# Optimization experiments

Measured on AMD Instinct MI355X. Metric: run time of the kernel, lower is better.

The kernel has to match this reference:

```python
import jax, jax.numpy as jnp
import numpy as np

D_STATE = 2048
D_INPUT = 64
KERNEL_SIZE = 16384


def setup_inputs() -> dict:
    key = jax.random.key(0)
    k_rad, k_ph, k_w = jax.random.split(key, 3)
    # Discrete diagonal state matrix: complex eigenvalues with radius in
    # [strong_stability, weak_stability] = [0.9, 0.999], uniform phase.
    radius = 0.9 + 0.099 * jax.random.uniform(k_rad, (D_STATE,), dtype=jnp.float32)
    phase = 2.0 * jnp.pi * jax.random.uniform(k_ph, (D_STATE,), dtype=jnp.float32)
    A = jnp.stack([radius * jnp.cos(phase), radius * jnp.sin(phase)], axis=-1)  # (P, 2) view_as_real
    # Reservoir uniform complex matrix W: (H, P) complex stored as (H, P, 2) real
    W = jax.random.uniform(k_w, (D_INPUT, D_STATE, 2), dtype=jnp.float32, minval=-1.0, maxval=1.0)
    return {"A": A, "W": W, "kernel_size": KERNEL_SIZE}


def reference(A, W, kernel_size):
    # view_as_complex
    Ac = A[:, 0] + 1j * A[:, 1]          # (P,)
    Wc = W[..., 0] + 1j * W[..., 1]      # (H, P)
    powers = jnp.arange(kernel_size, dtype=jnp.float32)  # (L,)
    # Vandermonde[j, l] = A[j]^l, computed stably in log-space (|A| < 1)
    vandermonde = jnp.exp(jnp.log(Ac)[:, None] * powers[None, :])  # (P, L) complex
    kernel = jnp.einsum('hp,pl->hl', Wc, vandermonde)  # (H, L) complex
    return kernel
```

## Files before the change

kernel.cpp:

```cpp
#include <hip/hip_runtime.h>
#include <hip/hip_bf16.h>
#include <stdint.h>

#define P 2048
#define HN 64
#define L 16384
#define BN 64
#define KTW 16

typedef __bf16 bf16_t;
typedef bf16_t bf16x8 __attribute__((ext_vector_type(8)));
typedef float f32x16 __attribute__((ext_vector_type(16)));

__device__ __forceinline__ float2 cmul(float2 a, float2 b) {
    return make_float2(a.x * b.x - a.y * b.y, a.x * b.y + a.y * b.x);
}

__device__ __forceinline__ uint32_t packbf(float2 v) {
    union { __hip_bfloat162 v; uint32_t u; } cv;
    cv.v = __float22bfloat162_rn(make_float2(v.x, v.y));
    return cv.u;
}

__global__ void mv_prep(const float* __restrict__ Win,
                        const float* __restrict__ Ain,
                        uint4* __restrict__ wexp,
                        float2* __restrict__ tcol,
                        float2* __restrict__ a32) {
    int gid = blockIdx.x * 256 + threadIdx.x;
    {
        int lane = gid & 63;
        int mt = (gid >> 6) & 1;
        int q = (gid >> 7) & 1;
        int kt = gid >> 8;
        int m = mt * 32 + (lane & 31);
        int p0 = kt * 16 + q * 8 + (lane >> 5) * 4;
        const float4* wp = (const float4*)(Win + (size_t)(m * P + p0) * 2);
        float4 f0 = wp[0], f1 = wp[1];
        float re[4] = {f0.x, f0.z, f1.x, f1.z};
        float im[4] = {f0.y, f0.w, f1.y, f1.w};
        uint32_t o[4];
#pragma unroll
        for (int j = 0; j < 4; ++j)
            o[j] = packbf(make_float2(re[j], -im[j]));
        wexp[gid] = make_uint4(o[0], o[1], o[2], o[3]);
    }
    {
        int p = gid >> 4;
        int e = gid & 15;
        float2 a = *(const float2*)(Ain + 2 * p);
        float2 a2 = cmul(a, a);
        float2 r = make_float2(1.f, 0.f);
        float2 sq = a2;
#pragma unroll
        for (int b = 0; b < 4; ++b) {
            if ((e >> b) & 1) r = cmul(r, sq);
            sq = cmul(sq, sq);
        }
        float2 ro = cmul(r, a);
        tcol[(size_t)p * 32 + 2 * e] = r;
        tcol[(size_t)p * 32 + 2 * e + 1] = ro;
        if (e == 15) a32[p] = cmul(ro, a);
    }
}

struct StepRegs {
    uint4 a[2][2];
    float2 tv[8];
};

__global__ void __launch_bounds__(512, 2) mv_main(
    const float* __restrict__ Ain,
    const uint4* __restrict__ wexp,
    const float2* __restrict__ Tcol,
    const float2* __restrict__ A32,
    float* __restrict__ out) {
    __shared__ __align__(16) float ldsp[8192];

    const int t = threadIdx.x;
    const int bn = blockIdx.x;
    const int w = t >> 6;
    const int lw = t & 63;

    float2* Base0 = (float2*)ldsp;
    float2* Base1 = Base0 + P;

    {
        float e = (float)(BN * bn);
        const float2* Af2 = (const float2*)Ain;
#pragma unroll
        for (int j = 0; j < 4; ++j) {
            int p = t + 512 * j;
            float2 a = Af2[p];
            float logr = 0.5f * logf(a.x * a.x + a.y * a.y);
            float th = atan2f(a.y, a.x);
            float mag = expf(e * logr);
            float s, c;
            sincosf(e * th, &s, &c);
            float2 b0 = make_float2(mag * c, mag * s);
            Base0[p] = b0;
            Base1[p] = cmul(b0, A32[p]);
        }
    }
    __syncthreads();

    const int n = lw & 31;
    const int kh = lw >> 5;
    const int kt0 = w * KTW;
    const float2* tc = Tcol + n;
    const float4* B0f4 = (const float4*)Base0;
    const float4* B1f4 = (const float4*)Base1;

    f32x16 acc[2][2];
#pragma unroll
    for (int mt = 0; mt < 2; ++mt)
#pragma unroll
        for (int nt = 0; nt < 2; ++nt)
#pragma unroll
            for (int r = 0; r < 16; ++r) acc[mt][nt][r] = 0.f;

    StepRegs s0, s1;

    auto load_step = [&](int kt, StepRegs& s) {
#pragma unroll
        for (int q = 0; q < 2; ++q) {
#pragma unroll
            for (int mt = 0; mt < 2; ++mt)
                s.a[mt][q] = wexp[(size_t)(((kt * 2 + q) * 2 + mt) * 64 + lw)];
            int pb = kt * 16 + q * 8 + kh * 4;
#pragma unroll
            for (int j = 0; j < 4; ++j)
                s.tv[q * 4 + j] = tc[(size_t)(pb + j) * 32];
        }
    };

    auto compute_step = [&](int kt, const StepRegs& s) {
#pragma unroll
        for (int q = 0; q < 2; ++q) {
            int bi = kt * 8 + q * 4 + kh * 2;
            float4 c0 = B0f4[bi], c1 = B0f4[bi + 1];
            float4 d0 = B1f4[bi], d1 = B1f4[bi + 1];
            float2 bb[4] = {make_float2(c0.x, c0.y), make_float2(c0.z, c0.w),
                            make_float2(c1.x, c1.y), make_float2(c1.z, c1.w)};
            float2 dd[4] = {make_float2(d0.x, d0.y), make_float2(d0.z, d0.w),
                            make_float2(d1.x, d1.y), make_float2(d1.z, d1.w)};
            uint32_t f0[4], f1[4];
#pragma unroll
            for (int j = 0; j < 4; ++j) {
                float2 tvv = s.tv[q * 4 + j];
                f0[j] = packbf(cmul(bb[j], tvv));
                f1[j] = packbf(cmul(dd[j], tvv));
            }
            union { uint4 u; bf16x8 v; } F0, F1, A0, A1;
            F0.u = make_uint4(f0[0], f0[1], f0[2], f0[3]);
            F1.u = make_uint4(f1[0], f1[1], f1[2], f1[3]);
            A0.u = s.a[0][q];
            A1.u = s.a[1][q];
            acc[0][0] = __builtin_amdgcn_mfma_f32_32x32x16_bf16(A0.v, F0.v, acc[0][0], 0, 0, 0);
            acc[1][0] = __builtin_amdgcn_mfma_f32_32x32x16_bf16(A1.v, F0.v, acc[1][0], 0, 0, 0);
            acc[0][1] = __builtin_amdgcn_mfma_f32_32x32x16_bf16(A0.v, F1.v, acc[0][1], 0, 0, 0);
            acc[1][1] = __builtin_amdgcn_mfma_f32_32x32x16_bf16(A1.v, F1.v, acc[1][1], 0, 0, 0);
        }
    };

    load_step(kt0, s0);
#pragma unroll
    for (int i = 0; i < KTW; i += 2) {
        if (i + 1 < KTW) load_step(kt0 + i + 1, s1);
        compute_step(kt0 + i, s0);
        if (i + 2 < KTW) load_step(kt0 + i + 2, s0);
        if (i + 1 < KTW) compute_step(kt0 + i + 1, s1);
    }

    __syncthreads();
    float* Red = ldsp;
    const int row = t >> 4;
    const int colb = (t & 15) * 2;
    const int rr = (row & 3) | ((row >> 3) << 2);
    const int lane0 = colb + ((row >> 2) & 1) * 32;

#pragma unroll
    for (int mt = 0; mt < 2; ++mt)
#pragma unroll
        for (int nt = 0; nt < 2; ++nt) {
#pragma unroll
            for (int r = 0; r < 16; ++r)
                Red[w * 1024 + r * 64 + lw] = acc[mt][nt][r];
            __syncthreads();
            float sx = 0.f, sy = 0.f;
#pragma unroll
            for (int ww = 0; ww < 8; ++ww) {
                sx += Red[ww * 1024 + rr * 64 + lane0];
                sy += Red[ww * 1024 + rr * 64 + lane0 + 1];
            }
            float2 o2 = make_float2(sx, sy);
            *(float2*)(out + (size_t)(mt * 32 + row) * L + (size_t)bn * BN + nt * 32 + colb) = o2;
            __syncthreads();
        }
}

extern "C" void kernel_launch(void* const* d_in, const int* in_sizes, int n_in,
                              void* d_out, int out_size, void* d_ws, size_t ws_size,
                              hipStream_t stream) {
    const float* Ain = nullptr;
    const float* Win = nullptr;
    for (int i = 0; i < n_in; ++i) {
        if (in_sizes[i] == 2 * P) Ain = (const float*)d_in[i];
        else if (in_sizes[i] == 2 * HN * P) Win = (const float*)d_in[i];
    }
    if (!Ain) Ain = (const float*)d_in[0];
    if (!Win) Win = (const float*)d_in[1];
    (void)out_size; (void)ws_size;
    uint4* wexp = (uint4*)d_ws;
    float2* tcol = (float2*)((char*)d_ws + 512 * 1024);
    float2* a32 = (float2*)((char*)d_ws + 1024 * 1024);
    mv_prep<<<128, 256, 0, stream>>>(Win, Ain, wexp, tcol, a32);
    mv_main<<<L / BN, 512, 0, stream>>>(Ain, wexp, tcol, a32, (float*)d_out);
}
```

Measured before the change: 81.10 us.

## Split P across blocks, keep W and T in registers, add partial-sum reduce

```diff
diff --git a/kernel.cpp b/kernel.cpp
--- a/kernel.cpp
+++ b/kernel.cpp
@@ -6,7 +6,10 @@
 #define HN 64
 #define L 16384
 #define BN 64
-#define KTW 16
+#define NT 4
+#define KQ 4
+#define KTWV 4
+#define HL (HN * L)
 
 typedef __bf16 bf16_t;
 typedef bf16_t bf16x8 __attribute__((ext_vector_type(8)));
@@ -26,7 +29,8 @@
                         const float* __restrict__ Ain,
                         uint4* __restrict__ wexp,
                         float2* __restrict__ tcol,
-                        float2* __restrict__ a32) {
+                        float2* __restrict__ a32,
+                        float2* __restrict__ a64) {
     int gid = blockIdx.x * 256 + threadIdx.x;
     {
         int lane = gid & 63;
@@ -60,143 +64,161 @@
         float2 ro = cmul(r, a);
         tcol[(size_t)p * 32 + 2 * e] = r;
         tcol[(size_t)p * 32 + 2 * e + 1] = ro;
-        if (e == 15) a32[p] = cmul(ro, a);
-    }
-}
-
-struct StepRegs {
-    uint4 a[2][2];
-    float2 tv[8];
-};
+        if (e == 15) {
+            float2 v32 = cmul(ro, a);
+            a32[p] = v32;
+            a64[p] = cmul(v32, v32);
+        }
+    }
+}
 
 __global__ void __launch_bounds__(512, 2) mv_main(
     const float* __restrict__ Ain,
     const uint4* __restrict__ wexp,
     const float2* __restrict__ Tcol,
     const float2* __restrict__ A32,
-    float* __restrict__ out) {
-    __shared__ __align__(16) float ldsp[8192];
+    const float2* __restrict__ A64,
+    float* __restrict__ part) {
+    __shared__ __align__(16) float2 Base0[512];
+    __shared__ __align__(16) float2 Base1[512];
+    __shared__ float Red[8][2][1024];
 
     const int t = threadIdx.x;
-    const int bn = blockIdx.x;
+    const int kq = blockIdx.x & 3;
+    const int cg = blockIdx.x >> 2;
     const int w = t >> 6;
     const int lw = t & 63;
-
-    float2* Base0 = (float2*)ldsp;
-    float2* Base1 = Base0 + P;
-
-    {
-        float e = (float)(BN * bn);
-        const float2* Af2 = (const float2*)Ain;
-#pragma unroll
-        for (int j = 0; j < 4; ++j) {
-            int p = t + 512 * j;
-            float2 a = Af2[p];
-            float logr = 0.5f * logf(a.x * a.x + a.y * a.y);
-            float th = atan2f(a.y, a.x);
-            float mag = expf(e * logr);
-            float s, c;
-            sincosf(e * th, &s, &c);
-            float2 b0 = make_float2(mag * c, mag * s);
-            Base0[p] = b0;
-            Base1[p] = cmul(b0, A32[p]);
-        }
-    }
-    __syncthreads();
-
     const int n = lw & 31;
     const int kh = lw >> 5;
-    const int kt0 = w * KTW;
-    const float2* tc = Tcol + n;
+
+    uint4 wreg[KTWV][2][2];
+    float2 tv[KTWV][8];
+    {
+        const float2* tc = Tcol + n;
+#pragma unroll
+        for (int kk = 0; kk < KTWV; ++kk) {
+            int kt = kq * 32 + w * 4 + kk;
+#pragma unroll
+            for (int q = 0; q < 2; ++q) {
+#pragma unroll
+                for (int mt = 0; mt < 2; ++mt)
+                    wreg[kk][mt][q] = wexp[(size_t)(((kt * 2 + q) * 2 + mt) * 64 + lw)];
+                int pb = kt * 16 + q * 8 + kh * 4;
+#pragma unroll
+                for (int jj = 0; jj < 4; ++jj)
+                    tv[kk][q * 4 + jj] = tc[(size_t)(pb + jj) * 32];
+            }
+        }
+    }
+
+    float2 a64v;
+    {
+        int p = kq * 512 + t;
+        float2 a = ((const float2*)Ain)[p];
+        float e = (float)(cg * 256);
+        float logr = 0.5f * logf(a.x * a.x + a.y * a.y);
+        float th = atan2f(a.y, a.x);
+        float mag = expf(e * logr);
+        float s, c;
+        sincosf(e * th, &s, &c);
+        float2 b0 = make_float2(mag * c, mag * s);
+        Base0[t] = b0;
+        Base1[t] = cmul(b0, A32[p]);
+        a64v = A64[p];
+    }
+    __syncthreads();
+
     const float4* B0f4 = (const float4*)Base0;
     const float4* B1f4 = (const float4*)Base1;
 
-    f32x16 acc[2][2];
-#pragma unroll
-    for (int mt = 0; mt < 2; ++mt)
-#pragma unroll
-        for (int nt = 0; nt < 2; ++nt)
-#pragma unroll
-            for (int r = 0; r < 16; ++r) acc[mt][nt][r] = 0.f;
-
-    StepRegs s0, s1;
-
-    auto load_step = [&](int kt, StepRegs& s) {
-#pragma unroll
-        for (int q = 0; q < 2; ++q) {
-#pragma unroll
-            for (int mt = 0; mt < 2; ++mt)
-                s.a[mt][q] = wexp[(size_t)(((kt * 2 + q) * 2 + mt) * 64 + lw)];
-            int pb = kt * 16 + q * 8 + kh * 4;
-#pragma unroll
-            for (int j = 0; j < 4; ++j)
-                s.tv[q * 4 + j] = tc[(size_t)(pb + j) * 32];
-        }
-    };
-
-    auto compute_step = [&](int kt, const StepRegs& s) {
-#pragma unroll
-        for (int q = 0; q < 2; ++q) {
-            int bi = kt * 8 + q * 4 + kh * 2;
-            float4 c0 = B0f4[bi], c1 = B0f4[bi + 1];
-            float4 d0 = B1f4[bi], d1 = B1f4[bi + 1];
-            float2 bb[4] = {make_float2(c0.x, c0.y), make_float2(c0.z, c0.w),
-                            make_float2(c1.x, c1.y), make_float2(c1.z, c1.w)};
-            float2 dd[4] = {make_float2(d0.x, d0.y), make_float2(d0.z, d0.w),
-                            make_float2(d1.x, d1.y), make_float2(d1.z, d1.w)};
-            uint32_t f0[4], f1[4];
-#pragma unroll
-            for (int j = 0; j < 4; ++j) {
-                float2 tvv = s.tv[q * 4 + j];
-                f0[j] = packbf(cmul(bb[j], tvv));
-                f1[j] = packbf(cmul(dd[j], tvv));
-            }
-            union { uint4 u; bf16x8 v; } F0, F1, A0, A1;
-            F0.u = make_uint4(f0[0], f0[1], f0[2], f0[3]);
-            F1.u = make_uint4(f1[0], f1[1], f1[2], f1[3]);
-            A0.u = s.a[0][q];
-            A1.u = s.a[1][q];
-            acc[0][0] = __builtin_amdgcn_mfma_f32_32x32x16_bf16(A0.v, F0.v, acc[0][0], 0, 0, 0);
-            acc[1][0] = __builtin_amdgcn_mfma_f32_32x32x16_bf16(A1.v, F0.v, acc[1][0], 0, 0, 0);
-            acc[0][1] = __builtin_amdgcn_mfma_f32_32x32x16_bf16(A0.v, F1.v, acc[0][1], 0, 0, 0);
-            acc[1][1] = __builtin_amdgcn_mfma_f32_32x32x16_bf16(A1.v, F1.v, acc[1][1], 0, 0, 0);
-        }
-    };
-
-    load_step(kt0, s0);
-#pragma unroll
-    for (int i = 0; i < KTW; i += 2) {
-        if (i + 1 < KTW) load_step(kt0 + i + 1, s1);
-        compute_step(kt0 + i, s0);
-        if (i + 2 < KTW) load_step(kt0 + i + 2, s0);
-        if (i + 1 < KTW) compute_step(kt0 + i + 1, s1);
-    }
-
-    __syncthreads();
-    float* Red = ldsp;
     const int row = t >> 4;
     const int colb = (t & 15) * 2;
     const int rr = (row & 3) | ((row >> 3) << 2);
     const int lane0 = colb + ((row >> 2) & 1) * 32;
 
-#pragma unroll
-    for (int mt = 0; mt < 2; ++mt)
-#pragma unroll
-        for (int nt = 0; nt < 2; ++nt) {
-#pragma unroll
-            for (int r = 0; r < 16; ++r)
-                Red[w * 1024 + r * 64 + lw] = acc[mt][nt][r];
+    for (int j = 0; j < NT; ++j) {
+        f32x16 acc[2][2];
+#pragma unroll
+        for (int mt = 0; mt < 2; ++mt)
+#pragma unroll
+            for (int nt = 0; nt < 2; ++nt)
+#pragma unroll
+                for (int r = 0; r < 16; ++r) acc[mt][nt][r] = 0.f;
+
+#pragma unroll
+        for (int kk = 0; kk < KTWV; ++kk) {
+#pragma unroll
+            for (int q = 0; q < 2; ++q) {
+                int bi = (4 * w + kk) * 8 + q * 4 + kh * 2;
+                float4 c0 = B0f4[bi], c1 = B0f4[bi + 1];
+                float4 d0 = B1f4[bi], d1 = B1f4[bi + 1];
+                uint32_t f0[4], f1[4];
+                {
+                    float2 tvv;
+                    tvv = tv[kk][q * 4 + 0];
+                    f0[0] = packbf(cmul(make_float2(c0.x, c0.y), tvv));
+                    f1[0] = packbf(cmul(make_float2(d0.x, d0.y), tvv));
+                    tvv = tv[kk][q * 4 + 1];
+                    f0[1] = packbf(cmul(make_float2(c0.z, c0.w), tvv));
+                    f1[1] = packbf(cmul(make_float2(d0.z, d0.w), tvv));
+                    tvv = tv[kk][q * 4 + 2];
+                    f0[2] = packbf(cmul(make_float2(c1.x, c1.y), tvv));
+                    f1[2] = packbf(cmul(make_float2(d1.x, d1.y), tvv));
+                    tvv = tv[kk][q * 4 + 3];
+                    f0[3] = packbf(cmul(make_float2(c1.z, c1.w), tvv));
+                    f1[3] = packbf(cmul(make_float2(d1.z, d1.w), tvv));
+                }
+                union { uint4 u; bf16x8 v; } F0, F1, A0, A1;
+                F0.u = make_uint4(f0[0], f0[1], f0[2], f0[3]);
+                F1.u = make_uint4(f1[0], f1[1], f1[2], f1[3]);
+                A0.u = wreg[kk][0][q];
+                A1.u = wreg[kk][1][q];
+                acc[0][0] = __builtin_amdgcn_mfma_f32_32x32x16_bf16(A0.v, F0.v, acc[0][0], 0, 0, 0);
+                acc[1][0] = __builtin_amdgcn_mfma_f32_32x32x16_bf16(A1.v, F0.v, acc[1][0], 0, 0, 0);
+                acc[0][1] = __builtin_amdgcn_mfma_f32_32x32x16_bf16(A0.v, F1.v, acc[0][1], 0, 0, 0);
+                acc[1][1] = __builtin_amdgcn_mfma_f32_32x32x16_bf16(A1.v, F1.v, acc[1][1], 0, 0, 0);
+            }
+        }
+
+#pragma unroll
+        for (int mt = 0; mt < 2; ++mt) {
+#pragma unroll
+            for (int nt = 0; nt < 2; ++nt)
+#pragma unroll
+                for (int r = 0; r < 16; ++r)
+                    Red[w][nt][r * 64 + lw] = acc[mt][nt][r];
             __syncthreads();
-            float sx = 0.f, sy = 0.f;
-#pragma unroll
-            for (int ww = 0; ww < 8; ++ww) {
-                sx += Red[ww * 1024 + rr * 64 + lane0];
-                sy += Red[ww * 1024 + rr * 64 + lane0 + 1];
+#pragma unroll
+            for (int nt = 0; nt < 2; ++nt) {
+                float sx = 0.f, sy = 0.f;
+#pragma unroll
+                for (int ww = 0; ww < 8; ++ww) {
+                    sx += Red[ww][nt][rr * 64 + lane0];
+                    sy += Red[ww][nt][rr * 64 + lane0 + 1];
+                }
+                *(float2*)(part + (size_t)kq * HL + (size_t)(mt * 32 + row) * L
+                           + cg * 256 + j * 64 + nt * 32 + colb) = make_float2(sx, sy);
             }
-            float2 o2 = make_float2(sx, sy);
-            *(float2*)(out + (size_t)(mt * 32 + row) * L + (size_t)bn * BN + nt * 32 + colb) = o2;
             __syncthreads();
         }
+
+        if (j < NT - 1) {
+            Base0[t] = cmul(Base0[t], a64v);
+            Base1[t] = cmul(Base1[t], a64v);
+            __syncthreads();
+        }
+    }
+}
+
+__global__ void mv_reduce(const float4* __restrict__ part,
+                          float4* __restrict__ out) {
+    int i = blockIdx.x * 256 + threadIdx.x;
+    float4 a = part[i];
+    float4 b = part[i + (HL / 4)];
+    float4 c = part[i + 2 * (HL / 4)];
+    float4 d = part[i + 3 * (HL / 4)];
+    out[i] = make_float4(a.x + b.x + c.x + d.x, a.y + b.y + c.y + d.y,
+                         a.z + b.z + c.z + d.z, a.w + b.w + c.w + d.w);
 }
 
 extern "C" void kernel_launch(void* const* d_in, const int* in_sizes, int n_in,
@@ -214,6 +236,9 @@
     uint4* wexp = (uint4*)d_ws;
     float2* tcol = (float2*)((char*)d_ws + 512 * 1024);
     float2* a32 = (float2*)((char*)d_ws + 1024 * 1024);
-    mv_prep<<<128, 256, 0, stream>>>(Win, Ain, wexp, tcol, a32);
-    mv_main<<<L / BN, 512, 0, stream>>>(Ain, wexp, tcol, a32, (float*)d_out);
-}
+    float2* a64 = (float2*)((char*)d_ws + 1040 * 1024);
+    float* part = (float*)((char*)d_ws + 2 * 1024 * 1024);
+    mv_prep<<<128, 256, 0, stream>>>(Win, Ain, wexp, tcol, a32, a64);
+    mv_main<<<256, 512, 0, stream>>>(Ain, wexp, tcol, a32, a64, part);
+    mv_reduce<<<1024, 256, 0, stream>>>((const float4*)part, (float4*)d_out);
+}
```

Result: slower. 89.73 us (+10.6%).

## Precompute per-block base powers in prep and split column halves across wave groups

Applied to the files above, without the earlier changes.

```diff
diff --git a/kernel.cpp b/kernel.cpp
--- a/kernel.cpp
+++ b/kernel.cpp
@@ -5,7 +5,6 @@
 #define P 2048
 #define HN 64
 #define L 16384
-#define BN 64
 #define KTW 16
 
 typedef __bf16 bf16_t;
@@ -26,7 +25,8 @@
                         const float* __restrict__ Ain,
                         uint4* __restrict__ wexp,
                         float2* __restrict__ tcol,
-                        float2* __restrict__ a32) {
+                        float2* __restrict__ a32,
+                        float2* __restrict__ abase) {
     int gid = blockIdx.x * 256 + threadIdx.x;
     {
         int lane = gid & 63;
@@ -62,66 +62,81 @@
         tcol[(size_t)p * 32 + 2 * e + 1] = ro;
         if (e == 15) a32[p] = cmul(ro, a);
     }
-}
-
-struct StepRegs {
+    {
+        int p = gid & 2047;
+        int j16 = gid >> 11;
+        float2 a = *(const float2*)(Ain + 2 * p);
+        float2 s = cmul(a, a);
+#pragma unroll
+        for (int i = 0; i < 5; ++i) s = cmul(s, s);
+        float2 a64v = s;
+        float2 t1k = a64v;
+#pragma unroll
+        for (int i = 0; i < 4; ++i) t1k = cmul(t1k, t1k);
+        float2 r = make_float2(1.f, 0.f);
+        float2 sq = t1k;
+#pragma unroll
+        for (int b = 0; b < 4; ++b) {
+            if ((j16 >> b) & 1) r = cmul(r, sq);
+            sq = cmul(sq, sq);
+        }
+        float2* ab = abase + (size_t)(j16 * 16) * P + p;
+#pragma unroll
+        for (int i = 0; i < 16; ++i) {
+            ab[(size_t)i * P] = r;
+            r = cmul(r, a64v);
+        }
+    }
+}
+
+struct Step {
     uint4 a[2][2];
     float2 tv[8];
 };
 
-__global__ void __launch_bounds__(512, 2) mv_main(
-    const float* __restrict__ Ain,
+__global__ void __launch_bounds__(1024, 4) mv_main(
     const uint4* __restrict__ wexp,
     const float2* __restrict__ Tcol,
     const float2* __restrict__ A32,
+    const float2* __restrict__ Abase,
     float* __restrict__ out) {
-    __shared__ __align__(16) float ldsp[8192];
+    __shared__ __align__(16) float lds[16384];
 
     const int t = threadIdx.x;
     const int bn = blockIdx.x;
     const int w = t >> 6;
     const int lw = t & 63;
-
-    float2* Base0 = (float2*)ldsp;
-    float2* Base1 = Base0 + P;
-
-    {
-        float e = (float)(BN * bn);
-        const float2* Af2 = (const float2*)Ain;
-#pragma unroll
-        for (int j = 0; j < 4; ++j) {
-            int p = t + 512 * j;
-            float2 a = Af2[p];
-            float logr = 0.5f * logf(a.x * a.x + a.y * a.y);
-            float th = atan2f(a.y, a.x);
-            float mag = expf(e * logr);
-            float s, c;
-            sincosf(e * th, &s, &c);
-            float2 b0 = make_float2(mag * c, mag * s);
-            Base0[p] = b0;
-            Base1[p] = cmul(b0, A32[p]);
-        }
-    }
-    __syncthreads();
-
+    const int g = w >> 3;
+    const int ks = w & 7;
     const int n = lw & 31;
     const int kh = lw >> 5;
-    const int kt0 = w * KTW;
+
+    float2* Base0 = (float2*)lds;
+    float2* Base1 = Base0 + P;
+
+    {
+        float4 ab = ((const float4*)(Abase + (size_t)bn * P))[t];
+        float4 a3 = ((const float4*)A32)[t];
+        float2 c0 = cmul(make_float2(ab.x, ab.y), make_float2(a3.x, a3.y));
+        float2 c1 = cmul(make_float2(ab.z, ab.w), make_float2(a3.z, a3.w));
+        ((float4*)Base0)[t] = ab;
+        ((float4*)Base1)[t] = make_float4(c0.x, c0.y, c1.x, c1.y);
+    }
+    __syncthreads();
+
+    const int kt0 = ks * KTW;
     const float2* tc = Tcol + n;
-    const float4* B0f4 = (const float4*)Base0;
-    const float4* B1f4 = (const float4*)Base1;
-
-    f32x16 acc[2][2];
+    const float4* Bg = (const float4*)(g ? Base1 : Base0);
+
+    f32x16 acc[2];
 #pragma unroll
     for (int mt = 0; mt < 2; ++mt)
 #pragma unroll
-        for (int nt = 0; nt < 2; ++nt)
-#pragma unroll
-            for (int r = 0; r < 16; ++r) acc[mt][nt][r] = 0.f;
-
-    StepRegs s0, s1;
-
-    auto load_step = [&](int kt, StepRegs& s) {
+        for (int r = 0; r < 16; ++r) acc[mt][r] = 0.f;
+
+    Step s0, s1;
+
+    auto load_step = [&](int kt, Step& s) {
 #pragma unroll
         for (int q = 0; q < 2; ++q) {
 #pragma unroll
@@ -134,32 +149,22 @@
         }
     };
 
-    auto compute_step = [&](int kt, const StepRegs& s) {
+    auto compute_step = [&](int kt, const Step& s) {
 #pragma unroll
         for (int q = 0; q < 2; ++q) {
             int bi = kt * 8 + q * 4 + kh * 2;
-            float4 c0 = B0f4[bi], c1 = B0f4[bi + 1];
-            float4 d0 = B1f4[bi], d1 = B1f4[bi + 1];
-            float2 bb[4] = {make_float2(c0.x, c0.y), make_float2(c0.z, c0.w),
-                            make_float2(c1.x, c1.y), make_float2(c1.z, c1.w)};
-            float2 dd[4] = {make_float2(d0.x, d0.y), make_float2(d0.z, d0.w),
-                            make_float2(d1.x, d1.y), make_float2(d1.z, d1.w)};
-            uint32_t f0[4], f1[4];
-#pragma unroll
-            for (int j = 0; j < 4; ++j) {
-                float2 tvv = s.tv[q * 4 + j];
-                f0[j] = packbf(cmul(bb[j], tvv));
-                f1[j] = packbf(cmul(dd[j], tvv));
-            }
-            union { uint4 u; bf16x8 v; } F0, F1, A0, A1;
-            F0.u = make_uint4(f0[0], f0[1], f0[2], f0[3]);
-            F1.u = make_uint4(f1[0], f1[1], f1[2], f1[3]);
+            float4 c0 = Bg[bi], c1 = Bg[bi + 1];
+            uint32_t f[4];
+            f[0] = packbf(cmul(make_float2(c0.x, c0.y), s.tv[q * 4 + 0]));
+            f[1] = packbf(cmul(make_float2(c0.z, c0.w), s.tv[q * 4 + 1]));
+            f[2] = packbf(cmul(make_float2(c1.x, c1.y), s.tv[q * 4 + 2]));
+            f[3] = packbf(cmul(make_float2(c1.z, c1.w), s.tv[q * 4 + 3]));
+            union { uint4 u; bf16x8 v; } F, A0, A1;
+            F.u = make_uint4(f[0], f[1], f[2], f[3]);
             A0.u = s.a[0][q];
             A1.u = s.a[1][q];
-            acc[0][0] = __builtin_amdgcn_mfma_f32_32x32x16_bf16(A0.v, F0.v, acc[0][0], 0, 0, 0);
-            acc[1][0] = __builtin_amdgcn_mfma_f32_32x32x16_bf16(A1.v, F0.v, acc[1][0], 0, 0, 0);
-            acc[0][1] = __builtin_amdgcn_mfma_f32_32x32x16_bf16(A0.v, F1.v, acc[0][1], 0, 0, 0);
-            acc[1][1] = __builtin_amdgcn_mfma_f32_32x32x16_bf16(A1.v, F1.v, acc[1][1], 0, 0, 0);
+            acc[0] = __builtin_amdgcn_mfma_f32_32x32x16_bf16(A0.v, F.v, acc[0], 0, 0, 0);
+            acc[1] = __builtin_amdgcn_mfma_f32_32x32x16_bf16(A1.v, F.v, acc[1], 0, 0, 0);
         }
     };
 
@@ -173,30 +178,31 @@
     }
 
     __syncthreads();
-    float* Red = ldsp;
-    const int row = t >> 4;
-    const int colb = (t & 15) * 2;
+    float* Red = lds;
+    const int tg = t & 511;
+    const int gr = t >> 9;
+    const int row = tg >> 4;
+    const int colb = (tg & 15) * 2;
     const int rr = (row & 3) | ((row >> 3) << 2);
     const int lane0 = colb + ((row >> 2) & 1) * 32;
 
 #pragma unroll
-    for (int mt = 0; mt < 2; ++mt)
-#pragma unroll
-        for (int nt = 0; nt < 2; ++nt) {
-#pragma unroll
-            for (int r = 0; r < 16; ++r)
-                Red[w * 1024 + r * 64 + lw] = acc[mt][nt][r];
-            __syncthreads();
-            float sx = 0.f, sy = 0.f;
-#pragma unroll
-            for (int ww = 0; ww < 8; ++ww) {
-                sx += Red[ww * 1024 + rr * 64 + lane0];
-                sy += Red[ww * 1024 + rr * 64 + lane0 + 1];
-            }
-            float2 o2 = make_float2(sx, sy);
-            *(float2*)(out + (size_t)(mt * 32 + row) * L + (size_t)bn * BN + nt * 32 + colb) = o2;
-            __syncthreads();
-        }
+    for (int mt = 0; mt < 2; ++mt) {
+#pragma unroll
+        for (int r = 0; r < 16; ++r)
+            Red[(g * 8 + ks) * 1024 + r * 64 + lw] = acc[mt][r];
+        __syncthreads();
+        float sx = 0.f, sy = 0.f;
+#pragma unroll
+        for (int ww = 0; ww < 8; ++ww) {
+            int base = (gr * 8 + ww) * 1024 + rr * 64 + lane0;
+            sx += Red[base];
+            sy += Red[base + 1];
+        }
+        *(float2*)(out + (size_t)(mt * 32 + row) * L + (size_t)bn * 64
+                   + gr * 32 + colb) = make_float2(sx, sy);
+        __syncthreads();
+    }
 }
 
 extern "C" void kernel_launch(void* const* d_in, const int* in_sizes, int n_in,
@@ -214,6 +220,7 @@
     uint4* wexp = (uint4*)d_ws;
     float2* tcol = (float2*)((char*)d_ws + 512 * 1024);
     float2* a32 = (float2*)((char*)d_ws + 1024 * 1024);
-    mv_prep<<<128, 256, 0, stream>>>(Win, Ain, wexp, tcol, a32);
-    mv_main<<<L / BN, 512, 0, stream>>>(Ain, wexp, tcol, a32, (float*)d_out);
-}
+    float2* abase = (float2*)((char*)d_ws + 2 * 1024 * 1024);
+    mv_prep<<<128, 256, 0, stream>>>(Win, Ain, wexp, tcol, a32, abase);
+    mv_main<<<256, 1024, 0, stream>>>(wexp, tcol, a32, abase, (float*)d_out);
+}
```

Measured after the change: 88.11 us. 1.09x slower.
